# Kernel tuning notes

Hardware: AMD Instinct MI355X
Metric: run time of the kernel (lower is better)

The kernel has to match this reference:

```python
import jax, jax.numpy as jnp
import numpy as np


def _grid_sample_bilinear(img, grid):
    # img: [B,C,H,W]; grid: [B,Hg,Wg,2] normalized to [-1,1] (x,y), align_corners=False,
    # zero padding (torch F.grid_sample defaults).
    B, C, H, W = img.shape
    Hg, Wg = grid.shape[1], grid.shape[2]
    gx, gy = grid[..., 0], grid[..., 1]
    ix = (gx + 1.0) * (W * 0.5) - 0.5
    iy = (gy + 1.0) * (H * 0.5) - 0.5
    ix0 = jnp.floor(ix)
    iy0 = jnp.floor(iy)
    tx = (ix - ix0).reshape(B, 1, -1)
    ty = (iy - iy0).reshape(B, 1, -1)
    img_flat = img.reshape(B, C, H * W)

    def corner(xi, yi):
        valid = ((xi >= 0) & (xi < W) & (yi >= 0) & (yi < H)).reshape(B, 1, -1)
        xc = jnp.clip(xi, 0, W - 1).astype(jnp.int32)
        yc = jnp.clip(yi, 0, H - 1).astype(jnp.int32)
        idx = (yc * W + xc).reshape(B, -1)                      # [B, Hg*Wg]
        vals = jax.vmap(lambda f, i: f[:, i])(img_flat, idx)    # [B, C, Hg*Wg]
        return vals * valid

    v00 = corner(ix0, iy0)
    v01 = corner(ix0 + 1, iy0)
    v10 = corner(ix0, iy0 + 1)
    v11 = corner(ix0 + 1, iy0 + 1)
    out = (v00 * (1 - tx) * (1 - ty) + v01 * tx * (1 - ty)
           + v10 * (1 - tx) * ty + v11 * tx * ty)
    return out.reshape(B, C, Hg, Wg)


def setup_inputs() -> dict:
    key = jax.random.key(0)
    ks = jax.random.split(key, 8)
    B, C, RHO, WP = 32, 384, 25, 256
    HC, WC = 64, 64
    D = 2 * C  # 768, channels after polar/cart concat
    std = 0.02
    return {
        "polar_feat": jax.random.normal(ks[0], (B, C, RHO, WP), jnp.float32),
        "cart_feat": jax.random.normal(ks[1], (B, C, HC, WC), jnp.float32),
        "grid": jax.random.uniform(ks[2], (B, RHO, WP, 2), jnp.float32, -1.0, 1.0),
        "W1_0": jax.random.normal(ks[3], (D, 40), jnp.float32) * std,
        "b1_0": jnp.zeros((40,), jnp.float32),
        "W2_0": jax.random.normal(ks[4], (40, 1), jnp.float32) * std,
        "b2_0": jnp.zeros((1,), jnp.float32),
        "W1s": jax.random.normal(ks[5], (24, D + 1, 40), jnp.float32) * std,
        "b1s": jnp.zeros((24, 40), jnp.float32),
        "W2s": jax.random.normal(ks[6], (24, 40, 1), jnp.float32) * std,
        "b2s": jnp.zeros((24, 1), jnp.float32),
    }


def reference(polar_feat, cart_feat, grid, W1_0, b1_0, W2_0, b2_0, W1s, b1s, W2s, b2s):
    # Polar grid-sample fusion of cartesian features onto the polar grid.
    fe_cart_p = _grid_sample_bilinear(cart_feat, grid)              # [B,C,25,Wp]
    fe_cat_p = jnp.concatenate([polar_feat, fe_cart_p], axis=1)     # [B,768,25,Wp]
    # AdaptiveAvgPool2d((None,1)): mean over width.
    fe = jnp.mean(fe_cat_p, axis=3)                                 # [B,768,25]

    feats = jnp.transpose(fe, (2, 0, 1))                            # [25,B,768]
    gelu = lambda x: jax.nn.gelu(x, approximate=False)

    # Head 0: no recurrent input.
    h0 = gelu(feats[0] @ W1_0 + b1_0)
    out0 = h0 @ W2_0 + b2_0                                         # [B,1]

    # Heads 1..24: concat previous scalar output before first linear (fully_local=False).
    def step(out_prev, xs):
        feat, W1, b1, W2, b2 = xs
        x = jnp.concatenate([feat, out_prev], axis=-1)              # [B,769]
        h = gelu(x @ W1 + b1)
        o = h @ W2 + b2                                             # [B,1]
        return o, o

    _, outs = jax.lax.scan(step, out0, (feats[1:], W1s, b1s, W2s, b2s))
    out = jnp.concatenate([out0[None], outs], axis=0)               # [25,B,1]
    out = jnp.transpose(out[:, :, 0], (1, 0))                       # [B,25]
    return jnp.clip(out, 0.0, jnp.pi)
```

## Files before the change

### kernel.cpp

```cpp
#include <hip/hip_runtime.h>
#include <math.h>

#define B_    32
#define C_    384
#define RHO_  25
#define WP_   256
#define PIX_  4096
#define D_    768
#define HID_  40
#define NROWS (B_*C_*RHO_)
#define FE_N (RHO_*B_*D_)
#define POLARBLK 2048

__device__ __forceinline__ float gelu_exact(float x) {
    return 0.5f * x * (1.f + erff(x * 0.70710678118654752f));
}

__global__ __launch_bounds__(256) void prep_kernel(const float* __restrict__ grid,
        const float* __restrict__ W1_0, const float* __restrict__ W1s,
        float* __restrict__ bins, float* __restrict__ W1T, float* __restrict__ fe) {
    __shared__ float lb[PIX_];
    int tid = threadIdx.x;
    if (blockIdx.x < B_ * RHO_) {
        for (int i = tid; i < PIX_ / 4; i += 256) ((float4*)lb)[i] = make_float4(0.f, 0.f, 0.f, 0.f);
        __syncthreads();
        int pt = blockIdx.x * WP_ + tid;
        float2 g = ((const float2*)grid)[pt];
        float ix = (g.x + 1.f) * 32.f - 0.5f;
        float iy = (g.y + 1.f) * 32.f - 0.5f;
        float x0f = floorf(ix), y0f = floorf(iy);
        float fx = ix - x0f, fy = iy - y0f;
        int x0 = (int)x0f, y0 = (int)y0f;
        const float s = 1.f / 256.f;
        if ((unsigned)x0 < 64u) {
            if ((unsigned)y0 < 64u)       atomicAdd(&lb[y0 * 64 + x0],       (1.f - fx) * (1.f - fy) * s);
            if ((unsigned)(y0 + 1) < 64u) atomicAdd(&lb[(y0 + 1) * 64 + x0], (1.f - fx) * fy * s);
        }
        if ((unsigned)(x0 + 1) < 64u) {
            if ((unsigned)y0 < 64u)       atomicAdd(&lb[y0 * 64 + x0 + 1],       fx * (1.f - fy) * s);
            if ((unsigned)(y0 + 1) < 64u) atomicAdd(&lb[(y0 + 1) * 64 + x0 + 1], fx * fy * s);
        }
        __syncthreads();
        float4* dst = (float4*)(bins + (size_t)blockIdx.x * PIX_);
        for (int i = tid; i < PIX_ / 4; i += 256) dst[i] = ((float4*)lb)[i];
    } else if (blockIdx.x < B_ * RHO_ + 25) {
        int i = blockIdx.x - B_ * RHO_;
        const float* src = (i == 0) ? W1_0 : (W1s + (size_t)(i - 1) * 769 * HID_);
        float* dst = W1T + (size_t)i * HID_ * D_;
        for (int idx = tid; idx < HID_ * D_; idx += 256) {
            int j = idx / D_, c = idx % D_;
            dst[idx] = src[c * HID_ + j];
        }
    } else {
        int z = blockIdx.x - (B_ * RHO_ + 25);
        float4* f4 = (float4*)fe;
        int per = FE_N / 4 / 50;
        for (int i = tid; i < per; i += 256)
            f4[z * per + i] = make_float4(0.f, 0.f, 0.f, 0.f);
    }
}

__global__ __launch_bounds__(256) void polar_mean_kernel(const float* __restrict__ polar,
                                                         float* __restrict__ fe) {
    int wid = blockIdx.x * 4 + (threadIdx.x >> 6);
    int lane = threadIdx.x & 63;
    const int NW = POLARBLK * 4;
    for (int r0 = wid; r0 < NROWS; r0 += 4 * NW) {
        float s[4];
        #pragma unroll
        for (int k = 0; k < 4; ++k) {
            int r = r0 + k * NW;
            float4 v = (r < NROWS) ? ((const float4*)(polar + (size_t)r * WP_))[lane]
                                   : make_float4(0.f, 0.f, 0.f, 0.f);
            s[k] = v.x + v.y + v.z + v.w;
        }
        #pragma unroll
        for (int m = 32; m >= 1; m >>= 1) {
            #pragma unroll
            for (int k = 0; k < 4; ++k) s[k] += __shfl_xor(s[k], m, 64);
        }
        if (lane == 0) {
            #pragma unroll
            for (int k = 0; k < 4; ++k) {
                int r = r0 + k * NW;
                if (r < NROWS) {
                    int rho = r % RHO_, cch = (r / RHO_) % C_, bb = r / (RHO_ * C_);
                    fe[((size_t)(rho * B_ + bb)) * D_ + cch] = s[k] * (1.f / 256.f);
                }
            }
        }
    }
}

__global__ __launch_bounds__(256) void cart_lds_kernel(const float* __restrict__ cart,
        const float* __restrict__ bins, float* __restrict__ fe) {
    __shared__ float ldsW[6400];
    int tid = threadIdx.x;
    int bid = blockIdx.x;
    int b   = bid / 192;
    int rem = bid % 192;
    int ct  = rem >> 4;
    int pc  = rem & 15;

    {
        const float4* binb4 = (const float4*)(bins + (size_t)b * RHO_ * PIX_ + pc * 256);
        float4* lw4 = (float4*)ldsW;
        #pragma unroll 2
        for (int i = tid; i < 1600; i += 256) {
            int r = i >> 6, e = i & 63;
            lw4[(r << 6) + e] = binb4[(size_t)r * 1024 + e];
        }
    }
    __syncthreads();

    int w = tid >> 6, lane = tid & 63;
    int j = lane >> 3, q = lane & 7;
    int c = ct * 32 + w * 8 + j;
    const float* xp = cart + ((size_t)b * C_ + c) * PIX_ + pc * 256 + q * 4;

    float acc[25];
    #pragma unroll
    for (int r = 0; r < 25; ++r) acc[r] = 0.f;

    float4 x0 = *(const float4*)(xp);
    float4 x1 = *(const float4*)(xp + 32);
    for (int t = 0; t < 8; ++t) {
        float4 xc = x0;
        x0 = x1;
        if (t < 6) x1 = *(const float4*)(xp + (t + 2) * 32);
        const float* wb = ldsW + t * 32 + q * 4;
        #pragma unroll
        for (int r = 0; r < 25; ++r) {
            float4 wv = *(const float4*)(wb + (r << 8));
            acc[r] += xc.x * wv.x + xc.y * wv.y + xc.z * wv.z + xc.w * wv.w;
        }
    }
    #pragma unroll
    for (int r = 0; r < 25; ++r) {
        acc[r] += __shfl_xor(acc[r], 1, 64);
        acc[r] += __shfl_xor(acc[r], 2, 64);
        acc[r] += __shfl_xor(acc[r], 4, 64);
    }
    if (q == 0) {
        #pragma unroll
        for (int r = 0; r < 25; ++r)
            atomicAdd(&fe[((size_t)(r * B_ + b)) * D_ + 384 + c], acc[r]);
    }
}

__global__ __launch_bounds__(256) void mlp_pre_kernel(const float* __restrict__ fe,
        const float* __restrict__ W1T, const float* __restrict__ b1_0,
        const float* __restrict__ b1s, float* __restrict__ G) {
    int lane = threadIdx.x & 63;
    int trip = blockIdx.x * 4 + (threadIdx.x >> 6);
    int jh = trip & 1;
    int pair = trip >> 1;
    int i = pair >> 5, b = pair & 31;
    const float4* f4p = (const float4*)(fe + (size_t)(i * B_ + b) * D_);
    float4 f0 = f4p[lane], f1 = f4p[lane + 64], f2 = f4p[lane + 128];
    int j0 = jh * 20;
    #pragma unroll 2
    for (int j = j0; j < j0 + 20; ++j) {
        const float4* w4p = (const float4*)(W1T + ((size_t)i * HID_ + j) * D_);
        float4 w0 = w4p[lane], w1 = w4p[lane + 64], w2 = w4p[lane + 128];
        float s = f0.x*w0.x + f0.y*w0.y + f0.z*w0.z + f0.w*w0.w
                + f1.x*w1.x + f1.y*w1.y + f1.z*w1.z + f1.w*w1.w
                + f2.x*w2.x + f2.y*w2.y + f2.z*w2.z + f2.w*w2.w;
        #pragma unroll
        for (int m = 32; m >= 1; m >>= 1) s += __shfl_xor(s, m, 64);
        if (lane == 0) {
            float bias = (i == 0) ? b1_0[j] : b1s[(i - 1) * HID_ + j];
            G[(size_t)(i * B_ + b) * HID_ + j] = s + bias;
        }
    }
}

__global__ __launch_bounds__(64) void mlp_seq_kernel(const float* __restrict__ G,
        const float* __restrict__ W1s, const float* __restrict__ W2_0,
        const float* __restrict__ b2_0, const float* __restrict__ W2s,
        const float* __restrict__ b2s, float* __restrict__ out) {
    int lane = threadIdx.x;
    int j2 = lane & 31, b = blockIdx.x * 2 + (lane >> 5);
    bool hi = (j2 < 8);
    float g1[25], g2[25], wl1[25], wl2[25], w2a[25], w2b[25], bsc[25];
    #pragma unroll
    for (int i = 0; i < 25; ++i) {
        g1[i] = G[(size_t)(i * B_ + b) * HID_ + j2];
        g2[i] = hi ? G[(size_t)(i * B_ + b) * HID_ + 32 + j2] : 0.f;
    }
    wl1[0] = 0.f; wl2[0] = 0.f;
    w2a[0] = W2_0[j2]; w2b[0] = hi ? W2_0[32 + j2] : 0.f; bsc[0] = b2_0[0];
    #pragma unroll
    for (int i = 1; i < 25; ++i) {
        size_t base = ((size_t)(i - 1) * 769 + 768) * HID_;
        wl1[i] = W1s[base + j2];
        wl2[i] = hi ? W1s[base + 32 + j2] : 0.f;
        w2a[i] = W2s[(i - 1) * HID_ + j2];
        w2b[i] = hi ? W2s[(i - 1) * HID_ + 32 + j2] : 0.f;
        bsc[i] = b2s[i - 1];
    }
    float op = 0.f;
    #pragma unroll
    for (int i = 0; i < 25; ++i) {
        float x1 = g1[i] + op * wl1[i];
        float x2 = g2[i] + op * wl2[i];
        float p = gelu_exact(x1) * w2a[i] + gelu_exact(x2) * w2b[i];
        #pragma unroll
        for (int m = 16; m >= 1; m >>= 1) p += __shfl_xor(p, m, 64);
        float o = p + bsc[i];
        op = o;
        if (j2 == 0) out[b * 25 + i] = fminf(fmaxf(o, 0.f), 3.14159265358979323846f);
    }
}

extern "C" void kernel_launch(void* const* d_in, const int* in_sizes, int n_in,
                              void* d_out, int out_size, void* d_ws, size_t ws_size,
                              hipStream_t stream) {
    const float* polar = (const float*)d_in[0];
    const float* cart  = (const float*)d_in[1];
    const float* grid  = (const float*)d_in[2];
    const float* W1_0  = (const float*)d_in[3];
    const float* b1_0  = (const float*)d_in[4];
    const float* W2_0  = (const float*)d_in[5];
    const float* b2_0  = (const float*)d_in[6];
    const float* W1s   = (const float*)d_in[7];
    const float* b1s   = (const float*)d_in[8];
    const float* W2s   = (const float*)d_in[9];
    const float* b2s   = (const float*)d_in[10];
    float* out = (float*)d_out;

    float* bins = (float*)d_ws;
    float* fe   = bins + (size_t)B_ * RHO_ * PIX_;
    float* G    = fe + (size_t)FE_N;
    float* W1T  = G + (size_t)RHO_ * B_ * HID_;

    prep_kernel<<<B_ * RHO_ + 25 + 50, 256, 0, stream>>>(grid, W1_0, W1s, bins, W1T, fe);
    polar_mean_kernel<<<POLARBLK, 256, 0, stream>>>(polar, fe);
    cart_lds_kernel<<<B_ * 12 * 16, 256, 0, stream>>>(cart, bins, fe);
    mlp_pre_kernel<<<(RHO_ * B_ * 2) / 4, 256, 0, stream>>>(fe, W1T, b1_0, b1s, G);
    mlp_seq_kernel<<<B_ / 2, 64, 0, stream>>>(G, W1s, W2_0, b2_0, W2s, b2s, out);
}
```

Baseline: 206.5 us.

## Fuse polar mean and cartesian projection into one interleaved kernel

Merges the polar width-mean kernel and the cartesian LDS projection kernel into a single launch. Block indices are interleaved so three of every four groups do cartesian work and one does polar rows, letting both memory-bound streams overlap. Each cartesian thread now handles two channels (c and c+32), so every LDS weight load feeds twice as many FMAs. This doubles the accumulator registers, which may reduce occupancy, and the polar work is now a fixed 75 rows per wave.

```diff
diff --git a/kernel.cpp b/kernel.cpp
--- a/kernel.cpp
+++ b/kernel.cpp
@@ -10,7 +10,6 @@
 #define HID_  40
 #define NROWS (B_*C_*RHO_)
 #define FE_N (RHO_*B_*D_)
-#define POLARBLK 2048
 
 __device__ __forceinline__ float gelu_exact(float x) {
     return 0.5f * x * (1.f + erff(x * 0.70710678118654752f));
@@ -60,91 +59,103 @@
     }
 }
 
-__global__ __launch_bounds__(256) void polar_mean_kernel(const float* __restrict__ polar,
-                                                         float* __restrict__ fe) {
-    int wid = blockIdx.x * 4 + (threadIdx.x >> 6);
-    int lane = threadIdx.x & 63;
-    const int NW = POLARBLK * 4;
-    for (int r0 = wid; r0 < NROWS; r0 += 4 * NW) {
-        float s[4];
-        #pragma unroll
-        for (int k = 0; k < 4; ++k) {
-            int r = r0 + k * NW;
-            float4 v = (r < NROWS) ? ((const float4*)(polar + (size_t)r * WP_))[lane]
-                                   : make_float4(0.f, 0.f, 0.f, 0.f);
-            s[k] = v.x + v.y + v.z + v.w;
-        }
-        #pragma unroll
-        for (int m = 32; m >= 1; m >>= 1) {
-            #pragma unroll
-            for (int k = 0; k < 4; ++k) s[k] += __shfl_xor(s[k], m, 64);
-        }
-        if (lane == 0) {
-            #pragma unroll
-            for (int k = 0; k < 4; ++k) {
-                int r = r0 + k * NW;
-                if (r < NROWS) {
-                    int rho = r % RHO_, cch = (r / RHO_) % C_, bb = r / (RHO_ * C_);
+__global__ __launch_bounds__(256) void main_kernel(const float* __restrict__ polar,
+        const float* __restrict__ cart, const float* __restrict__ bins,
+        float* __restrict__ fe) {
+    __shared__ float ldsW[6400];
+    int tid = threadIdx.x;
+    int lane = tid & 63, w = tid >> 6;
+    int o = blockIdx.x >> 3, sub = blockIdx.x & 7;
+
+    if ((o & 3) != 3) {
+        int bid = ((o >> 2) * 3 + (o & 3)) * 8 + sub;
+        int b   = bid / 96;
+        int rem = bid % 96;
+        int ct  = rem >> 4;
+        int pc  = rem & 15;
+
+        {
+            const float4* binb4 = (const float4*)(bins + (size_t)b * RHO_ * PIX_ + pc * 256);
+            float4* lw4 = (float4*)ldsW;
+            #pragma unroll 2
+            for (int i = tid; i < 1600; i += 256) {
+                int r = i >> 6, e = i & 63;
+                lw4[(r << 6) + e] = binb4[(size_t)r * 1024 + e];
+            }
+        }
+        __syncthreads();
+
+        int j = lane >> 3, q = lane & 7;
+        int c0 = ct * 64 + w * 8 + j;
+        const float* xp0 = cart + ((size_t)b * C_ + c0) * PIX_ + pc * 256 + q * 4;
+        const float* xp1 = xp0 + (size_t)32 * PIX_;
+
+        float acc0[25], acc1[25];
+        #pragma unroll
+        for (int r = 0; r < 25; ++r) { acc0[r] = 0.f; acc1[r] = 0.f; }
+
+        float4 a0 = *(const float4*)(xp0);
+        float4 a1 = *(const float4*)(xp0 + 32);
+        float4 b0 = *(const float4*)(xp1);
+        float4 b1 = *(const float4*)(xp1 + 32);
+        for (int t = 0; t < 8; ++t) {
+            float4 xa = a0, xb = b0;
+            a0 = a1; b0 = b1;
+            if (t < 6) {
+                a1 = *(const float4*)(xp0 + (t + 2) * 32);
+                b1 = *(const float4*)(xp1 + (t + 2) * 32);
+            }
+            const float* wb = ldsW + t * 32 + q * 4;
+            #pragma unroll
+            for (int r = 0; r < 25; ++r) {
+                float4 wv = *(const float4*)(wb + (r << 8));
+                acc0[r] += xa.x * wv.x + xa.y * wv.y + xa.z * wv.z + xa.w * wv.w;
+                acc1[r] += xb.x * wv.x + xb.y * wv.y + xb.z * wv.z + xb.w * wv.w;
+            }
+        }
+        #pragma unroll
+        for (int r = 0; r < 25; ++r) {
+            acc0[r] += __shfl_xor(acc0[r], 1, 64);
+            acc0[r] += __shfl_xor(acc0[r], 2, 64);
+            acc0[r] += __shfl_xor(acc0[r], 4, 64);
+            acc1[r] += __shfl_xor(acc1[r], 1, 64);
+            acc1[r] += __shfl_xor(acc1[r], 2, 64);
+            acc1[r] += __shfl_xor(acc1[r], 4, 64);
+        }
+        if (q == 0) {
+            #pragma unroll
+            for (int r = 0; r < 25; ++r) {
+                float* fr = fe + ((size_t)(r * B_ + b)) * D_ + 384;
+                atomicAdd(fr + c0,      acc0[r]);
+                atomicAdd(fr + c0 + 32, acc1[r]);
+            }
+        }
+    } else {
+        int pid = (o >> 2) * 8 + sub;
+        int wid = pid * 4 + w;
+        int r0 = wid * 75;
+        for (int it = 0; it < 15; ++it) {
+            int r = r0 + it * 5;
+            float s[5];
+            #pragma unroll
+            for (int k = 0; k < 5; ++k) {
+                float4 v = ((const float4*)(polar + (size_t)(r + k) * WP_))[lane];
+                s[k] = v.x + v.y + v.z + v.w;
+            }
+            #pragma unroll
+            for (int m = 32; m >= 1; m >>= 1) {
+                #pragma unroll
+                for (int k = 0; k < 5; ++k) s[k] += __shfl_xor(s[k], m, 64);
+            }
+            if (lane == 0) {
+                #pragma unroll
+                for (int k = 0; k < 5; ++k) {
+                    int rr = r + k;
+                    int rho = rr % RHO_, cch = (rr / RHO_) % C_, bb = rr / (RHO_ * C_);
                     fe[((size_t)(rho * B_ + bb)) * D_ + cch] = s[k] * (1.f / 256.f);
                 }
             }
         }
-    }
-}
-
-__global__ __launch_bounds__(256) void cart_lds_kernel(const float* __restrict__ cart,
-        const float* __restrict__ bins, float* __restrict__ fe) {
-    __shared__ float ldsW[6400];
-    int tid = threadIdx.x;
-    int bid = blockIdx.x;
-    int b   = bid / 192;
-    int rem = bid % 192;
-    int ct  = rem >> 4;
-    int pc  = rem & 15;
-
-    {
-        const float4* binb4 = (const float4*)(bins + (size_t)b * RHO_ * PIX_ + pc * 256);
-        float4* lw4 = (float4*)ldsW;
-        #pragma unroll 2
-        for (int i = tid; i < 1600; i += 256) {
-            int r = i >> 6, e = i & 63;
-            lw4[(r << 6) + e] = binb4[(size_t)r * 1024 + e];
-        }
-    }
-    __syncthreads();
-
-    int w = tid >> 6, lane = tid & 63;
-    int j = lane >> 3, q = lane & 7;
-    int c = ct * 32 + w * 8 + j;
-    const float* xp = cart + ((size_t)b * C_ + c) * PIX_ + pc * 256 + q * 4;
-
-    float acc[25];
-    #pragma unroll
-    for (int r = 0; r < 25; ++r) acc[r] = 0.f;
-
-    float4 x0 = *(const float4*)(xp);
-    float4 x1 = *(const float4*)(xp + 32);
-    for (int t = 0; t < 8; ++t) {
-        float4 xc = x0;
-        x0 = x1;
-        if (t < 6) x1 = *(const float4*)(xp + (t + 2) * 32);
-        const float* wb = ldsW + t * 32 + q * 4;
-        #pragma unroll
-        for (int r = 0; r < 25; ++r) {
-            float4 wv = *(const float4*)(wb + (r << 8));
-            acc[r] += xc.x * wv.x + xc.y * wv.y + xc.z * wv.z + xc.w * wv.w;
-        }
-    }
-    #pragma unroll
-    for (int r = 0; r < 25; ++r) {
-        acc[r] += __shfl_xor(acc[r], 1, 64);
-        acc[r] += __shfl_xor(acc[r], 2, 64);
-        acc[r] += __shfl_xor(acc[r], 4, 64);
-    }
-    if (q == 0) {
-        #pragma unroll
-        for (int r = 0; r < 25; ++r)
-            atomicAdd(&fe[((size_t)(r * B_ + b)) * D_ + 384 + c], acc[r]);
     }
 }
 
@@ -235,8 +246,7 @@
     float* W1T  = G + (size_t)RHO_ * B_ * HID_;
 
     prep_kernel<<<B_ * RHO_ + 25 + 50, 256, 0, stream>>>(grid, W1_0, W1s, bins, W1T, fe);
-    polar_mean_kernel<<<POLARBLK, 256, 0, stream>>>(polar, fe);
-    cart_lds_kernel<<<B_ * 12 * 16, 256, 0, stream>>>(cart, bins, fe);
+    main_kernel<<<4096, 256, 0, stream>>>(polar, cart, bins, fe);
     mlp_pre_kernel<<<(RHO_ * B_ * 2) / 4, 256, 0, stream>>>(fe, W1T, b1_0, b1s, G);
     mlp_seq_kernel<<<B_ / 2, 64, 0, stream>>>(G, W1s, W2_0, b2_0, W2s, b2s, out);
 }
```

After: 213.3 us. 3.3% more time.

## Process four channel groups per thread in cart kernel to reuse LDS weights

Applied to the files above, without the earlier changes.

The cart projection kernel now has each thread handle four channels (strided by 32) instead of one, so each LDS weight float4 load is reused across four accumulators. The 25 rho rows are split into two passes of 13 and 12 to limit register pressure. The grid shrinks fourfold (1536 blocks), which cuts redundant staging of the bins tile into LDS. In exchange, each pass re-reads the cart input from global memory, and fewer blocks lowers parallelism.

```diff
diff --git a/kernel.cpp b/kernel.cpp
--- a/kernel.cpp
+++ b/kernel.cpp
@@ -92,13 +92,65 @@
     }
 }
 
-__global__ __launch_bounds__(256) void cart_lds_kernel(const float* __restrict__ cart,
+template<int R0, int NR>
+__device__ __forceinline__ void cart_pass(const float* __restrict__ xp0, const float* ldsW,
+                                          int q, float* __restrict__ feb, int b, int c0) {
+    const float* xp[4];
+    #pragma unroll
+    for (int s = 0; s < 4; ++s) xp[s] = xp0 + (size_t)32 * s * PIX_;
+
+    float acc[4][NR];
+    #pragma unroll
+    for (int s = 0; s < 4; ++s)
+        #pragma unroll
+        for (int r = 0; r < NR; ++r) acc[s][r] = 0.f;
+
+    float4 cur[4], nxt[4];
+    #pragma unroll
+    for (int s = 0; s < 4; ++s) { cur[s] = *(const float4*)(xp[s]); nxt[s] = *(const float4*)(xp[s] + 32); }
+
+    for (int t = 0; t < 8; ++t) {
+        float4 xc[4];
+        #pragma unroll
+        for (int s = 0; s < 4; ++s) { xc[s] = cur[s]; cur[s] = nxt[s]; }
+        if (t < 6) {
+            #pragma unroll
+            for (int s = 0; s < 4; ++s) nxt[s] = *(const float4*)(xp[s] + (t + 2) * 32);
+        }
+        const float* wb = ldsW + t * 32 + q * 4;
+        #pragma unroll
+        for (int r = 0; r < NR; ++r) {
+            float4 wv = *(const float4*)(wb + ((R0 + r) << 8));
+            #pragma unroll
+            for (int s = 0; s < 4; ++s)
+                acc[s][r] += xc[s].x * wv.x + xc[s].y * wv.y + xc[s].z * wv.z + xc[s].w * wv.w;
+        }
+    }
+    #pragma unroll
+    for (int s = 0; s < 4; ++s)
+        #pragma unroll
+        for (int r = 0; r < NR; ++r) {
+            acc[s][r] += __shfl_xor(acc[s][r], 1, 64);
+            acc[s][r] += __shfl_xor(acc[s][r], 2, 64);
+            acc[s][r] += __shfl_xor(acc[s][r], 4, 64);
+        }
+    if (q == 0) {
+        #pragma unroll
+        for (int r = 0; r < NR; ++r) {
+            float* fr = feb + ((size_t)((R0 + r) * B_ + b)) * D_ + 384 + c0;
+            #pragma unroll
+            for (int s = 0; s < 4; ++s) atomicAdd(fr + 32 * s, acc[s][r]);
+        }
+    }
+}
+
+__global__ __launch_bounds__(256) void cart_kernel(const float* __restrict__ cart,
         const float* __restrict__ bins, float* __restrict__ fe) {
     __shared__ float ldsW[6400];
     int tid = threadIdx.x;
     int bid = blockIdx.x;
-    int b   = bid / 192;
-    int rem = bid % 192;
+    int b   = bid / 48;
+    int rem = bid % 48;
     int ct  = rem >> 4;
     int pc  = rem & 15;
 
@@ -115,37 +167,11 @@
 
     int w = tid >> 6, lane = tid & 63;
     int j = lane >> 3, q = lane & 7;
-    int c = ct * 32 + w * 8 + j;
-    const float* xp = cart + ((size_t)b * C_ + c) * PIX_ + pc * 256 + q * 4;
-
-    float acc[25];
-    #pragma unroll
-    for (int r = 0; r < 25; ++r) acc[r] = 0.f;
-
-    float4 x0 = *(const float4*)(xp);
-    float4 x1 = *(const float4*)(xp + 32);
-    for (int t = 0; t < 8; ++t) {
-        float4 xc = x0;
-        x0 = x1;
-        if (t < 6) x1 = *(const float4*)(xp + (t + 2) * 32);
-        const float* wb = ldsW + t * 32 + q * 4;
-        #pragma unroll
-        for (int r = 0; r < 25; ++r) {
-            float4 wv = *(const float4*)(wb + (r << 8));
-            acc[r] += xc.x * wv.x + xc.y * wv.y + xc.z * wv.z + xc.w * wv.w;
-        }
-    }
-    #pragma unroll
-    for (int r = 0; r < 25; ++r) {
-        acc[r] += __shfl_xor(acc[r], 1, 64);
-        acc[r] += __shfl_xor(acc[r], 2, 64);
-        acc[r] += __shfl_xor(acc[r], 4, 64);
-    }
-    if (q == 0) {
-        #pragma unroll
-        for (int r = 0; r < 25; ++r)
-            atomicAdd(&fe[((size_t)(r * B_ + b)) * D_ + 384 + c], acc[r]);
-    }
+    int c0 = ct * 128 + w * 8 + j;
+    const float* xp0 = cart + ((size_t)b * C_ + c0) * PIX_ + pc * 256 + q * 4;
+
+    cart_pass<0, 13>(xp0, ldsW, q, fe, b, c0);
+    cart_pass<13, 12>(xp0, ldsW, q, fe, b, c0);
 }
 
 __global__ __launch_bounds__(256) void mlp_pre_kernel(const float* __restrict__ fe,
@@ -236,7 +262,7 @@
 
     prep_kernel<<<B_ * RHO_ + 25 + 50, 256, 0, stream>>>(grid, W1_0, W1s, bins, W1T, fe);
     polar_mean_kernel<<<POLARBLK, 256, 0, stream>>>(polar, fe);
-    cart_lds_kernel<<<B_ * 12 * 16, 256, 0, stream>>>(cart, bins, fe);
+    cart_kernel<<<B_ * 3 * 16, 256, 0, stream>>>(cart, bins, fe);
     mlp_pre_kernel<<<(RHO_ * B_ * 2) / 4, 256, 0, stream>>>(fe, W1T, b1_0, b1s, G);
     mlp_seq_kernel<<<B_ / 2, 64, 0, stream>>>(G, W1s, W2_0, b2_0, W2s, b2s, out);
 }
```

Result: slower. 247.0 us (+19.6%).
